# Kernel tuning notes

Measured on AMD Instinct MI355X. Metric: run time of the kernel, lower is better.

## Reference

```python
import jax, jax.numpy as jnp
import numpy as np

H, KV, D, EPS = 32, 8, 128, 1e-6
G = H // KV  # kv groups = 4
ROPE_THETA = 5000000.0


def _rms_norm(x, gamma):
    # x: (..., D)
    return x * jax.lax.rsqrt(jnp.mean(x * x, axis=-1, keepdims=True) + EPS) * gamma


def _rotate_half(x):
    x1, x2 = jnp.split(x, 2, axis=-1)
    return jnp.concatenate([-x2, x1], axis=-1)


def _apply_rope(x, cos, sin):
    # x: (b, h, s, D); cos/sin: (b, s, 1, D) -> (b, 1, s, D)
    cos = jnp.transpose(cos, (0, 2, 1, 3))
    sin = jnp.transpose(sin, (0, 2, 1, 3))
    return x * cos + _rotate_half(x) * sin


def setup_inputs() -> dict:
    key = jax.random.key(0)
    ks = jax.random.split(key, 8)
    b, s, hid = 2, 2048, 2560
    hidden = jax.random.normal(ks[0], (b, s, hid), dtype=jnp.float32)
    # realistic RoPE tables (half-split convention matching _rotate_half)
    inv_freq = 1.0 / (ROPE_THETA ** (np.arange(0, D, 2, dtype=np.float32) / D))  # (D/2,)
    pos = np.arange(s, dtype=np.float32)
    freqs = np.outer(pos, inv_freq)                     # (s, D/2)
    emb = np.concatenate([freqs, freqs], axis=-1)       # (s, D)
    cos = jnp.broadcast_to(jnp.asarray(np.cos(emb))[None, :, None, :], (b, s, 1, D))
    sin = jnp.broadcast_to(jnp.asarray(np.sin(emb))[None, :, None, :], (b, s, 1, D))
    sc = 1.0 / np.sqrt(hid)
    wq = jax.random.normal(ks[1], (H * D, hid), dtype=jnp.float32) * sc
    wk = jax.random.normal(ks[2], (KV * D, hid), dtype=jnp.float32) * sc
    wv = jax.random.normal(ks[3], (KV * D, hid), dtype=jnp.float32) * sc
    wo = jax.random.normal(ks[4], (hid, H * D), dtype=jnp.float32) * (1.0 / np.sqrt(H * D))
    q_gamma = jnp.ones((D,), dtype=jnp.float32)
    k_gamma = jnp.ones((D,), dtype=jnp.float32)
    return {"hidden": hidden, "cos": cos, "sin": sin, "wq": wq, "wk": wk,
            "wv": wv, "wo": wo, "q_gamma": q_gamma, "k_gamma": k_gamma}


def reference(hidden, cos, sin, wq, wk, wv, wo, q_gamma, k_gamma):
    b, s, _ = hidden.shape
    # projections -> (b, heads, s, D)
    q = (hidden @ wq.T).reshape(b, s, H, D).transpose(0, 2, 1, 3)
    k = (hidden @ wk.T).reshape(b, s, KV, D).transpose(0, 2, 1, 3)
    v = (hidden @ wv.T).reshape(b, s, KV, D).transpose(0, 2, 1, 3)
    # QK-RMSNorm over head_dim
    q = _rms_norm(q, q_gamma)
    k = _rms_norm(k, k_gamma)
    # RoPE
    q = _apply_rope(q, cos, sin)
    k = _apply_rope(k, cos, sin)
    new_k, new_v = k, v  # kv cache (no prior cache)
    # GQA attention without materializing expanded K/V
    qg = q.reshape(b, KV, G, s, D)
    scale = 1.0 / np.sqrt(D)
    scores = jnp.einsum('bkgqd,bkld->bkgql', qg, k) * scale  # (b,KV,G,s,s)
    causal = jnp.tril(jnp.ones((s, s), dtype=bool))
    scores = jnp.where(causal, scores, jnp.finfo(scores.dtype).min)
    probs = jax.nn.softmax(scores, axis=-1)
    out = jnp.einsum('bkgql,bkld->bkgqd', probs, v)          # (b,KV,G,s,D)
    out = out.reshape(b, H, s, D).transpose(0, 2, 1, 3).reshape(b, s, H * D)
    return (out @ wo.T, new_k, new_v)
```

## Files before the change

kernel.cpp:

```cpp
#include <hip/hip_runtime.h>
#include <stdint.h>

typedef unsigned short u16;
typedef __attribute__((ext_vector_type(8))) short short8;
typedef __attribute__((ext_vector_type(4))) float f32x4;

#define MFMA_BF16(a,b,c) __builtin_amdgcn_mfma_f32_16x16x32_bf16((a),(b),(c),0,0,0)

#define S_BARRIER()  asm volatile("s_barrier" ::: "memory")
#define WAIT_LGKM0() asm volatile("s_waitcnt lgkmcnt(0)" ::: "memory")
#define WAIT_VM(N)   asm volatile("s_waitcnt vmcnt(" #N ")" ::: "memory")

__device__ __forceinline__ u16 f2bf(float x) {
    uint32_t u = __builtin_bit_cast(uint32_t, x);
    u += 0x7fffu + ((u >> 16) & 1u);
    return (u16)(u >> 16);
}
__device__ __forceinline__ float bf2f(u16 u) {
    return __builtin_bit_cast(float, (uint32_t)u << 16);
}
__device__ __forceinline__ void glds16(const void* g, void* lds) {
    __builtin_amdgcn_global_load_lds((const __attribute__((address_space(1))) void*)g,
                                     (__attribute__((address_space(3))) void*)lds,
                                     16, 0, 0);
}

__device__ __forceinline__ void cvt4(const float* __restrict__ s,
                                     u16* __restrict__ d, int i) {
    float4 v = *(const float4*)(s + i);
    ushort4 o;
    o.x = f2bf(v.x); o.y = f2bf(v.y); o.z = f2bf(v.z); o.w = f2bf(v.w);
    *(ushort4*)(d + i) = o;
}
__global__ __launch_bounds__(256) void cvt_all(
        const float* __restrict__ s0, u16* __restrict__ d0,
        const float* __restrict__ s1, u16* __restrict__ d1,
        const float* __restrict__ s2, u16* __restrict__ d2,
        const float* __restrict__ s3, u16* __restrict__ d3,
        const float* __restrict__ s4, u16* __restrict__ d4)
{
    int i = (blockIdx.x * 256 + threadIdx.x) * 4;
    if      (i < 10485760) cvt4(s0, d0, i);
    else if (i < 20971520) cvt4(s1, d1, i - 10485760);
    else if (i < 23592960) cvt4(s2, d2, i - 20971520);
    else if (i < 26214400) cvt4(s3, d3, i - 23592960);
    else if (i < 36700160) cvt4(s4, d4, i - 26214400);
}

template<int MH, int NH>
__device__ __forceinline__ void mm16(f32x4 (&acc)[8][4],
                                     const short8 (&a)[4][2],
                                     const short8 (&b)[2][2]) {
#pragma unroll
    for (int k2 = 0; k2 < 2; k2++)
#pragma unroll
        for (int mi = 0; mi < 4; mi++)
#pragma unroll
            for (int nj = 0; nj < 2; nj++)
                acc[MH * 4 + mi][NH * 2 + nj] =
                    MFMA_BF16(a[mi][k2], b[nj][k2], acc[MH * 4 + mi][NH * 2 + nj]);
}

template<bool BF16_OUT>
__global__ __launch_bounds__(512, 2) void gemm8(const u16* __restrict__ A,
                                                const u16* __restrict__ B,
                                                void* __restrict__ Cv,
                                                int K, int lda, int ldb, int ldc,
                                                int ntn)
{
    __shared__ __align__(16) u16 Sm[65536];
    const int t = threadIdx.x;
    const int w = t >> 6, l = t & 63;
    const int lrow = l & 15, lk = l >> 4;
    const int wm = w >> 2, wn = w & 3;

    const int nwg = (int)gridDim.x;
    const int cpx = nwg >> 3;
    const int id = (int)blockIdx.x;
    const int sw = (id & 7) * cpx + (id >> 3);
    const int tm = sw / ntn, tn = sw - tm * ntn;
    const int m0 = tm * 256, n0 = tn * 256;

    const int nkt = K >> 6;
    const size_t laneOffA = (size_t)(w * 16 + (l >> 3)) * lda + (((l & 7) ^ (l >> 3)) * 8);
    const size_t laneOffB = (size_t)(w * 16 + (l >> 3)) * ldb + (((l & 7) ^ (l >> 3)) * 8);
    const u16* Ag = A + (size_t)m0 * lda;
    const u16* Bg = B + (size_t)n0 * ldb;

    auto STAGE_A = [&](int kt, int slot, int h) {
#pragma unroll
        for (int j = 0; j < 2; j++)
            glds16(Ag + laneOffA + (size_t)(h * 128 + j * 8) * lda + kt * 64,
                   (char*)Sm + slot * 65536 + h * 16384 + w * 2048 + j * 1024);
    };
    auto STAGE_B = [&](int kt, int slot, int h) {
#pragma unroll
        for (int j = 0; j < 2; j++)
            glds16(Bg + laneOffB + (size_t)(h * 128 + j * 8) * ldb + kt * 64,
                   (char*)Sm + 32768 + slot * 65536 + h * 16384 + w * 2048 + j * 1024);
    };
    auto READ_A = [&](short8 (&a)[4][2], int slot, int rb) {
#pragma unroll
        for (int mi = 0; mi < 4; mi++)
#pragma unroll
            for (int k2 = 0; k2 < 2; k2++) {
                int row = rb + mi * 16 + lrow;
                a[mi][k2] = *(const short8*)&Sm[slot * 32768 + row * 64 +
                                                (((k2 * 4 + lk) ^ (lrow & 7)) * 8)];
            }
    };
    auto READ_B = [&](short8 (&b)[2][2], int slot, int rb) {
#pragma unroll
        for (int nj = 0; nj < 2; nj++)
#pragma unroll
            for (int k2 = 0; k2 < 2; k2++) {
                int row = rb + nj * 16 + lrow;
                b[nj][k2] = *(const short8*)&Sm[slot * 32768 + 16384 + row * 64 +
                                                (((k2 * 4 + lk) ^ (lrow & 7)) * 8)];
            }
    };

    f32x4 acc[8][4];
#pragma unroll
    for (int i = 0; i < 8; i++)
#pragma unroll
        for (int j = 0; j < 4; j++) acc[i][j] = (f32x4){0.f, 0.f, 0.f, 0.f};
    short8 aF0[4][2], aF1[4][2], bF0[2][2], bF1[2][2];

    STAGE_A(0, 0, 0); STAGE_A(0, 0, 1);
    STAGE_B(0, 0, 0); STAGE_B(0, 0, 1);
    const int k1 = (nkt > 1) ? 1 : 0;
    STAGE_A(k1, 1, 0); STAGE_A(k1, 1, 1);
    WAIT_VM(4);
    S_BARRIER();

    for (int kt = 0; kt < nkt; ++kt) {
        const int slot = kt & 1, nslot = slot ^ 1;
        const int ktB = (kt + 1 < nkt) ? kt + 1 : kt;
        const int ktA = (kt + 2 < nkt) ? kt + 2 : kt;
        READ_A(aF0, slot, wm * 128);
        READ_B(bF0, slot, wn * 64);
        STAGE_B(ktB, nslot, 0);
        S_BARRIER();
        WAIT_LGKM0();
        __builtin_amdgcn_sched_barrier(0);
        __builtin_amdgcn_s_setprio(1);
        mm16<0, 0>(acc, aF0, bF0);
        __builtin_amdgcn_s_setprio(0);
        S_BARRIER();
        READ_A(aF1, slot, wm * 128 + 64);
        STAGE_B(ktB, nslot, 1);
        S_BARRIER();
        WAIT_LGKM0();
        __builtin_amdgcn_sched_barrier(0);
        __builtin_amdgcn_s_setprio(1);
        mm16<1, 0>(acc, aF1, bF0);
        __builtin_amdgcn_s_setprio(0);
        S_BARRIER();
        READ_B(bF1, slot, wn * 64 + 32);
        STAGE_A(ktA, slot, 0);
        S_BARRIER();
        WAIT_LGKM0();
        __builtin_amdgcn_sched_barrier(0);
        __builtin_amdgcn_s_setprio(1);
        mm16<1, 1>(acc, aF1, bF1);
        __builtin_amdgcn_s_setprio(0);
        S_BARRIER();
        STAGE_A(ktA, slot, 1);
        S_BARRIER();
        __builtin_amdgcn_s_setprio(1);
        mm16<0, 1>(acc, aF0, bF1);
        __builtin_amdgcn_s_setprio(0);
        WAIT_VM(4);
        S_BARRIER();
    }
    WAIT_VM(0);

#pragma unroll
    for (int mi = 0; mi < 8; mi++) {
#pragma unroll
        for (int r = 0; r < 4; r++) {
            int row = m0 + wm * 128 + mi * 16 + lk * 4 + r;
#pragma unroll
            for (int nj = 0; nj < 4; nj++) {
                int col = n0 + wn * 64 + nj * 16 + lrow;
                float v = acc[mi][nj][r];
                if (BF16_OUT) ((u16*)Cv)[(size_t)row * ldc + col] = f2bf(v);
                else          ((float*)Cv)[(size_t)row * ldc + col] = v;
            }
        }
    }
}

__global__ __launch_bounds__(256) void norm_rope_qk(const u16* __restrict__ qkv,
        const float* __restrict__ cosb, const float* __restrict__ sinb,
        const float* __restrict__ qg, const float* __restrict__ kg,
        u16* __restrict__ qb, u16* __restrict__ kb, float* __restrict__ k_out)
{
    const int idx = blockIdx.x * 4 + (threadIdx.x >> 6);
    const int l = threadIdx.x & 63;
    const int tok = idx / 40, hd = idx - tok * 40;
    const int b = tok >> 11, pos = tok & 2047;
    const u16* row = qkv + (size_t)tok * 6144 + hd * 128;
    ushort2 xr = *(const ushort2*)(row + 2 * l);
    float xa = bf2f(xr.x), xb = bf2f(xr.y);
    float ss = xa * xa + xb * xb;
#pragma unroll
    for (int m = 1; m < 64; m <<= 1) ss += __shfl_xor(ss, m, 64);
    float rn = rsqrtf(ss * (1.0f / 128.0f) + 1e-6f);

    const float* gm = (hd < 32) ? qg : kg;
    float2 g = *(const float2*)(gm + 2 * l);
    float na = xa * rn * g.x, nb = xb * rn * g.y;
    float pa = __shfl_xor(na, 32, 64);
    float pb = __shfl_xor(nb, 32, 64);
    float2 c = *(const float2*)(cosb + (size_t)tok * 128 + 2 * l);
    float2 s = *(const float2*)(sinb + (size_t)tok * 128 + 2 * l);
    float sgn = (l < 32) ? -1.0f : 1.0f;
    float ya = na * c.x + sgn * pa * s.x;
    float yb = nb * c.y + sgn * pb * s.y;
    if (hd < 32) {
        const float qs = 0.12751745f;
        size_t base = (((size_t)b * 32 + hd) * 2048 + pos) * 128;
        ushort2 o; o.x = f2bf(ya * qs); o.y = f2bf(yb * qs);
        *(ushort2*)(qb + base + 2 * l) = o;
    } else {
        int kv = hd - 32;
        size_t base = (((size_t)b * 8 + kv) * 2048 + pos) * 128;
        *(float2*)(k_out + base + 2 * l) = make_float2(ya, yb);
        ushort2 o; o.x = f2bf(ya); o.y = f2bf(yb);
        *(ushort2*)(kb + base + 2 * l) = o;
    }
}

__global__ __launch_bounds__(256) void v_pack(const u16* __restrict__ qkv,
        float* __restrict__ v_out, u16* __restrict__ vtb)
{
    __shared__ __align__(16) u16 T[64 * 128];
    const int pb = blockIdx.x, bkv = blockIdx.y;
    const int b = bkv >> 3, kv = bkv & 7;
    const int p0 = pb * 64;
    const int t = threadIdx.x;
    const int pos = t >> 2, ch4 = t & 3;
    const u16* src = qkv + (size_t)(b * 2048 + p0 + pos) * 6144 + (40 + kv) * 128 + ch4 * 32;
    float* vdst = v_out + ((size_t)bkv * 2048 + p0 + pos) * 128 + ch4 * 32;
#pragma unroll
    for (int j = 0; j < 4; j++) {
        short8 x = *(const short8*)(src + j * 8);
        float4 f0, f1;
        f0.x = bf2f(x[0]); f0.y = bf2f(x[1]); f0.z = bf2f(x[2]); f0.w = bf2f(x[3]);
        f1.x = bf2f(x[4]); f1.y = bf2f(x[5]); f1.z = bf2f(x[6]); f1.w = bf2f(x[7]);
        *(float4*)(vdst + j * 8)     = f0;
        *(float4*)(vdst + j * 8 + 4) = f1;
        int slot = (ch4 * 4 + j) ^ (pos & 7);
        *(short8*)&T[pos * 128 + slot * 8] = x;
    }
    __syncthreads();
    const int d = t & 127, ph = t >> 7;
    u16* obase = vtb + ((size_t)bkv * 128 + d) * 2048 + p0 + ph * 32;
#pragma unroll
    for (int g = 0; g < 4; g++) {
        short8 tv;
#pragma unroll
        for (int jj = 0; jj < 8; jj++) {
            int pp = ph * 32 + g * 8 + jj;
            int slot = (d >> 3) ^ (pp & 7);
            tv[jj] = (short)T[pp * 128 + slot * 8 + (d & 7)];
        }
        *(short8*)(obase + g * 8) = tv;
    }
}

__global__ __launch_bounds__(256, 3) void attn_kernel(const u16* __restrict__ qb,
        const u16* __restrict__ kb, const u16* __restrict__ vtb,
        u16* __restrict__ ao)
{
    __shared__ __align__(16) u16 Ks[64 * 128];
    __shared__ __align__(16) u16 Vs[128 * 64];
    __shared__ __align__(16) u16 Ps[4][32 * 72];

    const int p = (int)blockIdx.x;
    const int g = (p & 7) + ((p >> 5) << 3);
    const int bh = g * 4 + ((p >> 3) & 3);
    const int b = bh >> 5, h = bh & 31;
    const int kvh = h >> 2;
    const int qt = (int)gridDim.y - 1 - (int)blockIdx.y;
    const int q0 = qt * 128;
    const int t = threadIdx.x, w = t >> 6, l = t & 63;
    const int lrow = l & 15, lk = l >> 4;

    const u16* qbase  = qb  + ((size_t)b * 32 + h)  * 2048 * 128;
    const u16* kbase  = kb  + ((size_t)b * 8 + kvh) * 2048 * 128;
    const u16* vtbase = vtb + ((size_t)b * 8 + kvh) * 128 * 2048;

    short8 qf[2][4];
#pragma unroll
    for (int m = 0; m < 2; m++) {
        const u16* qrow = qbase + (size_t)(q0 + w * 32 + m * 16 + lrow) * 128 + lk * 8;
#pragma unroll
        for (int ks = 0; ks < 4; ks++) qf[m][ks] = *(const short8*)(qrow + ks * 32);
    }

    f32x4 o[2][8];
#pragma unroll
    for (int m = 0; m < 2; m++)
#pragma unroll
        for (int i = 0; i < 8; i++) o[m][i] = (f32x4){0.f, 0.f, 0.f, 0.f};
    float lsum[2][4] = {{0.f,0.f,0.f,0.f},{0.f,0.f,0.f,0.f}};

    int kR[4], kG[4], vR[4], vG[4];
#pragma unroll
    for (int i = 0; i < 4; i++) {
        int c = i * 256 + t;
        kR[i] = c >> 4; kG[i] = (c & 15) ^ (kR[i] & 7);
        vR[i] = c >> 3; vG[i] = (c & 7)  ^ (vR[i] & 7);
    }
    char* Ksb = (char*)Ks + w * 1024;
    char* Vsb = (char*)Vs + w * 1024;
    u16* pw = &Ps[w][0];
    const int wrow_max = q0 + w * 32 + 31;

    const int nkt = 2 * qt + 2;
    for (int kt = 0; kt < nkt; kt++) {
        const int kv0 = kt * 64;
        const bool live = (kv0 <= wrow_max);

#pragma unroll
        for (int i = 0; i < 4; i++)
            glds16(kbase + (size_t)(kv0 + kR[i]) * 128 + kG[i] * 8, Ksb + i * 4096);
#pragma unroll
        for (int i = 0; i < 4; i++)
            glds16(vtbase + (size_t)vR[i] * 2048 + kv0 + vG[i] * 8, Vsb + i * 4096);

        WAIT_VM(4);
        S_BARRIER();

        f32x4 s[2][4];
        if (live) {
#pragma unroll
            for (int m = 0; m < 2; m++)
#pragma unroll
                for (int i = 0; i < 4; i++) s[m][i] = (f32x4){0.f, 0.f, 0.f, 0.f};
#pragma unroll
            for (int ks = 0; ks < 4; ks++) {
#pragma unroll
                for (int nt = 0; nt < 4; nt++) {
                    int r = nt * 16 + lrow;
                    int sl = (ks * 4 + lk) ^ (r & 7);
                    short8 kf = *(const short8*)&Ks[r * 128 + sl * 8];
                    s[0][nt] = MFMA_BF16(qf[0][ks], kf, s[0][nt]);
                    s[1][nt] = MFMA_BF16(qf[1][ks], kf, s[1][nt]);
                }
            }
#pragma unroll
            for (int m = 0; m < 2; m++) {
                const int rowbase = q0 + w * 32 + m * 16;
                if (kv0 + 63 > rowbase) {
#pragma unroll
                    for (int nt = 0; nt < 4; nt++) {
                        int cg = kv0 + nt * 16 + lrow;
#pragma unroll
                        for (int r = 0; r < 4; r++)
                            if (cg > rowbase + lk * 4 + r) s[m][nt][r] = -1e30f;
                    }
                }
#pragma unroll
                for (int nt = 0; nt < 4; nt++)
#pragma unroll
                    for (int r = 0; r < 4; r++) {
                        float pv = exp2f(s[m][nt][r]);
                        lsum[m][r] += pv;
                        pw[(m * 16 + lk * 4 + r) * 72 + nt * 16 + lrow] = f2bf(pv);
                    }
            }
            WAIT_LGKM0();
        }

        WAIT_VM(0);
        S_BARRIER();

        if (live) {
#pragma unroll
            for (int k2 = 0; k2 < 2; k2++) {
                short8 pf0 = *(const short8*)&pw[lrow * 72 + k2 * 32 + lk * 8];
                short8 pf1 = *(const short8*)&pw[(16 + lrow) * 72 + k2 * 32 + lk * 8];
#pragma unroll
                for (int nt = 0; nt < 8; nt++) {
                    int rr = nt * 16 + lrow;
                    int sl = (k2 * 4 + lk) ^ (rr & 7);
                    short8 vf = *(const short8*)&Vs[rr * 64 + sl * 8];
                    o[0][nt] = MFMA_BF16(pf0, vf, o[0][nt]);
                    o[1][nt] = MFMA_BF16(pf1, vf, o[1][nt]);
                }
            }
        }
        S_BARRIER();
    }

#pragma unroll
    for (int m = 0; m < 2; m++)
#pragma unroll
        for (int r = 0; r < 4; r++) {
            float v = lsum[m][r];
            v += __shfl_xor(v, 1, 64);
            v += __shfl_xor(v, 2, 64);
            v += __shfl_xor(v, 4, 64);
            v += __shfl_xor(v, 8, 64);
            lsum[m][r] = 1.0f / v;
        }
#pragma unroll
    for (int m = 0; m < 2; m++)
#pragma unroll
        for (int nt = 0; nt < 8; nt++)
#pragma unroll
            for (int r = 0; r < 4; r++) {
                int tok = q0 + w * 32 + m * 16 + lk * 4 + r;
                size_t off = ((size_t)b * 2048 + tok) * 4096 + h * 128 + nt * 16 + lrow;
                ao[off] = f2bf(o[m][nt][r] * lsum[m][r]);
            }
}

extern "C" void kernel_launch(void* const* d_in, const int* in_sizes, int n_in,
                              void* d_out, int out_size, void* d_ws, size_t ws_size,
                              hipStream_t stream)
{
    (void)in_sizes; (void)n_in; (void)out_size; (void)ws_size;
    const float* hidden = (const float*)d_in[0];
    const float* cosb   = (const float*)d_in[1];
    const float* sinb   = (const float*)d_in[2];
    const float* wq     = (const float*)d_in[3];
    const float* wk     = (const float*)d_in[4];
    const float* wv     = (const float*)d_in[5];
    const float* wo     = (const float*)d_in[6];
    const float* qg     = (const float*)d_in[7];
    const float* kg     = (const float*)d_in[8];

    float* out   = (float*)d_out;
    float* k_out = out + (size_t)2 * 2048 * 2560;
    float* v_out = k_out + (size_t)2 * 8 * 2048 * 128;

    u16* hid_b = (u16*)d_ws;
    u16* w_b   = hid_b + 10485760;
    u16* wo_b  = w_b   + 15728640;
    u16* q_b   = wo_b  + 10485760;
    u16* k_b   = q_b   + 16777216;
    u16* vt_b  = k_b   + 4194304;
    u16* qkv_b = vt_b  + 4194304;
    u16* ao_b  = hid_b;

    cvt_all<<<35840, 256, 0, stream>>>(hidden, hid_b, wq, w_b,
                                       wk, w_b + 10485760, wv, w_b + 13107200,
                                       wo, wo_b);

    gemm8<true><<<dim3(384), 512, 0, stream>>>(hid_b, w_b, qkv_b,
                                               2560, 2560, 2560, 6144, 24);
    norm_rope_qk<<<40960, 256, 0, stream>>>(qkv_b, cosb, sinb, qg, kg,
                                            q_b, k_b, k_out);
    v_pack<<<dim3(32, 16), 256, 0, stream>>>(qkv_b, v_out, vt_b);
    attn_kernel<<<dim3(64, 16), 256, 0, stream>>>(q_b, k_b, vt_b, ao_b);
    gemm8<false><<<dim3(160), 512, 0, stream>>>(ao_b, wo_b, out,
                                                4096, 4096, 4096, 2560, 10);
}
```

Measured before the change: 635.7 us.

## Replace output GEMM with simple 128x128 tile kernel and simplify attention loop

Adds a new single-buffered 128x128 tile GEMM (gemm_bt) for the output projection in place of the pipelined gemm8. It also simplifies attention synchronisation to plain __syncthreads with an early continue, and switches from exp2f to __expf with the Q prescale changed from log2e/sqrt(D) to 1/sqrt(D). The new GEMM drops the prefetch pipelining and uses smaller tiles, so load latency is exposed. The attention changes look more like a correctness or simplicity rewrite than a speedup.

```diff
diff --git a/kernel.cpp b/kernel.cpp
--- a/kernel.cpp
+++ b/kernel.cpp
@@ -185,6 +185,78 @@
             for (int nj = 0; nj < 4; nj++) {
                 int col = n0 + wn * 64 + nj * 16 + lrow;
                 float v = acc[mi][nj][r];
+                if (BF16_OUT) ((u16*)Cv)[(size_t)row * ldc + col] = f2bf(v);
+                else          ((float*)Cv)[(size_t)row * ldc + col] = v;
+            }
+        }
+    }
+}
+
+template<bool BF16_OUT>
+__global__ __launch_bounds__(256) void gemm_bt(const u16* __restrict__ A,
+                                               const u16* __restrict__ B,
+                                               void* __restrict__ Cv,
+                                               int K, int lda, int ldb, int ldc)
+{
+    __shared__ __align__(16) u16 As[128 * 64];
+    __shared__ __align__(16) u16 Bs[128 * 64];
+    const int t = threadIdx.x;
+    const int w = t >> 6, l = t & 63;
+    const int m0 = blockIdx.y * 128, n0 = blockIdx.x * 128;
+    const int wm = (w & 1) * 64, wn = (w >> 1) * 64;
+    const int lrow = l & 15, lk = l >> 4;
+
+    f32x4 acc[4][4];
+#pragma unroll
+    for (int i = 0; i < 4; i++)
+#pragma unroll
+        for (int j = 0; j < 4; j++) acc[i][j] = (f32x4){0.f, 0.f, 0.f, 0.f};
+
+    const int row_b = w * 8 + (l >> 3);
+    const int gsw = ((l & 7) ^ (l >> 3)) * 8;
+    const u16* Ap[4]; const u16* Bp[4];
+#pragma unroll
+    for (int i = 0; i < 4; i++) {
+        Ap[i] = A + (size_t)(m0 + row_b + i * 32) * lda + gsw;
+        Bp[i] = B + (size_t)(n0 + row_b + i * 32) * ldb + gsw;
+    }
+    char* Asb = (char*)As + w * 1024;
+    char* Bsb = (char*)Bs + w * 1024;
+
+    for (int k0 = 0; k0 < K; k0 += 64) {
+        __syncthreads();
+#pragma unroll
+        for (int i = 0; i < 4; i++) glds16(Ap[i] + k0, Asb + i * 4096);
+#pragma unroll
+        for (int i = 0; i < 4; i++) glds16(Bp[i] + k0, Bsb + i * 4096);
+        __syncthreads();
+#pragma unroll
+        for (int k2 = 0; k2 < 2; k2++) {
+            const int slb = (k2 * 4 + lk) ^ (lrow & 7);
+            short8 af[4], bf[4];
+#pragma unroll
+            for (int mi = 0; mi < 4; mi++)
+                af[mi] = *(const short8*)&As[(wm + mi * 16 + lrow) * 64 + slb * 8];
+#pragma unroll
+            for (int ni = 0; ni < 4; ni++)
+                bf[ni] = *(const short8*)&Bs[(wn + ni * 16 + lrow) * 64 + slb * 8];
+#pragma unroll
+            for (int mi = 0; mi < 4; mi++)
+#pragma unroll
+                for (int ni = 0; ni < 4; ni++)
+                    acc[mi][ni] = MFMA_BF16(af[mi], bf[ni], acc[mi][ni]);
+        }
+    }
+
+#pragma unroll
+    for (int mi = 0; mi < 4; mi++) {
+#pragma unroll
+        for (int r = 0; r < 4; r++) {
+            int row = m0 + wm + mi * 16 + lk * 4 + r;
+#pragma unroll
+            for (int ni = 0; ni < 4; ni++) {
+                int col = n0 + wn + ni * 16 + lrow;
+                float v = acc[mi][ni][r];
                 if (BF16_OUT) ((u16*)Cv)[(size_t)row * ldc + col] = f2bf(v);
                 else          ((float*)Cv)[(size_t)row * ldc + col] = v;
             }
@@ -220,7 +292,7 @@
     float ya = na * c.x + sgn * pa * s.x;
     float yb = nb * c.y + sgn * pb * s.y;
     if (hd < 32) {
-        const float qs = 0.12751745f;
+        const float qs = 0.08838834764831845f;
         size_t base = (((size_t)b * 32 + hd) * 2048 + pos) * 128;
         ushort2 o; o.x = f2bf(ya * qs); o.y = f2bf(yb * qs);
         *(ushort2*)(qb + base + 2 * l) = o;
@@ -323,78 +395,71 @@
     const int nkt = 2 * qt + 2;
     for (int kt = 0; kt < nkt; kt++) {
         const int kv0 = kt * 64;
-        const bool live = (kv0 <= wrow_max);
-
+        __syncthreads();
 #pragma unroll
         for (int i = 0; i < 4; i++)
             glds16(kbase + (size_t)(kv0 + kR[i]) * 128 + kG[i] * 8, Ksb + i * 4096);
 #pragma unroll
         for (int i = 0; i < 4; i++)
             glds16(vtbase + (size_t)vR[i] * 2048 + kv0 + vG[i] * 8, Vsb + i * 4096);
-
-        WAIT_VM(4);
-        S_BARRIER();
+        __syncthreads();
+
+        if (kv0 > wrow_max) continue;
 
         f32x4 s[2][4];
-        if (live) {
-#pragma unroll
-            for (int m = 0; m < 2; m++)
-#pragma unroll
-                for (int i = 0; i < 4; i++) s[m][i] = (f32x4){0.f, 0.f, 0.f, 0.f};
-#pragma unroll
-            for (int ks = 0; ks < 4; ks++) {
+#pragma unroll
+        for (int m = 0; m < 2; m++)
+#pragma unroll
+            for (int i = 0; i < 4; i++) s[m][i] = (f32x4){0.f, 0.f, 0.f, 0.f};
+#pragma unroll
+        for (int ks = 0; ks < 4; ks++) {
+#pragma unroll
+            for (int nt = 0; nt < 4; nt++) {
+                int r = nt * 16 + lrow;
+                int sl = (ks * 4 + lk) ^ (r & 7);
+                short8 kf = *(const short8*)&Ks[r * 128 + sl * 8];
+                s[0][nt] = MFMA_BF16(qf[0][ks], kf, s[0][nt]);
+                s[1][nt] = MFMA_BF16(qf[1][ks], kf, s[1][nt]);
+            }
+        }
+
+#pragma unroll
+        for (int m = 0; m < 2; m++) {
+            const int rowbase = q0 + w * 32 + m * 16;
+            if (kv0 + 63 > rowbase) {
 #pragma unroll
                 for (int nt = 0; nt < 4; nt++) {
-                    int r = nt * 16 + lrow;
-                    int sl = (ks * 4 + lk) ^ (r & 7);
-                    short8 kf = *(const short8*)&Ks[r * 128 + sl * 8];
-                    s[0][nt] = MFMA_BF16(qf[0][ks], kf, s[0][nt]);
-                    s[1][nt] = MFMA_BF16(qf[1][ks], kf, s[1][nt]);
+                    int cg = kv0 + nt * 16 + lrow;
+#pragma unroll
+                    for (int r = 0; r < 4; r++)
+                        if (cg > rowbase + lk * 4 + r) s[m][nt][r] = -1e30f;
                 }
             }
 #pragma unroll
-            for (int m = 0; m < 2; m++) {
-                const int rowbase = q0 + w * 32 + m * 16;
-                if (kv0 + 63 > rowbase) {
-#pragma unroll
-                    for (int nt = 0; nt < 4; nt++) {
-                        int cg = kv0 + nt * 16 + lrow;
-#pragma unroll
-                        for (int r = 0; r < 4; r++)
-                            if (cg > rowbase + lk * 4 + r) s[m][nt][r] = -1e30f;
-                    }
+            for (int nt = 0; nt < 4; nt++)
+#pragma unroll
+                for (int r = 0; r < 4; r++) {
+                    float pv = __expf(s[m][nt][r]);
+                    s[m][nt][r] = pv;
+                    lsum[m][r] += pv;
+                    pw[(m * 16 + lk * 4 + r) * 72 + nt * 16 + lrow] = f2bf(pv);
                 }
-#pragma unroll
-                for (int nt = 0; nt < 4; nt++)
-#pragma unroll
-                    for (int r = 0; r < 4; r++) {
-                        float pv = exp2f(s[m][nt][r]);
-                        lsum[m][r] += pv;
-                        pw[(m * 16 + lk * 4 + r) * 72 + nt * 16 + lrow] = f2bf(pv);
-                    }
-            }
-            WAIT_LGKM0();
-        }
-
-        WAIT_VM(0);
-        S_BARRIER();
-
-        if (live) {
-#pragma unroll
-            for (int k2 = 0; k2 < 2; k2++) {
-                short8 pf0 = *(const short8*)&pw[lrow * 72 + k2 * 32 + lk * 8];
-                short8 pf1 = *(const short8*)&pw[(16 + lrow) * 72 + k2 * 32 + lk * 8];
-#pragma unroll
-                for (int nt = 0; nt < 8; nt++) {
-                    int rr = nt * 16 + lrow;
-                    int sl = (k2 * 4 + lk) ^ (rr & 7);
-                    short8 vf = *(const short8*)&Vs[rr * 64 + sl * 8];
-                    o[0][nt] = MFMA_BF16(pf0, vf, o[0][nt]);
-                    o[1][nt] = MFMA_BF16(pf1, vf, o[1][nt]);
-                }
-            }
-        }
-        S_BARRIER();
+        }
+        asm volatile("s_waitcnt lgkmcnt(0)" ::: "memory");
+
+#pragma unroll
+        for (int k2 = 0; k2 < 2; k2++) {
+            short8 pf0 = *(const short8*)&pw[lrow * 72 + k2 * 32 + lk * 8];
+            short8 pf1 = *(const short8*)&pw[(16 + lrow) * 72 + k2 * 32 + lk * 8];
+#pragma unroll
+            for (int nt = 0; nt < 8; nt++) {
+                int rr = nt * 16 + lrow;
+                int sl = (k2 * 4 + lk) ^ (rr & 7);
+                short8 vf = *(const short8*)&Vs[rr * 64 + sl * 8];
+                o[0][nt] = MFMA_BF16(pf0, vf, o[0][nt]);
+                o[1][nt] = MFMA_BF16(pf1, vf, o[1][nt]);
+            }
+        }
     }
 
 #pragma unroll
@@ -458,6 +523,6 @@
                                             q_b, k_b, k_out);
     v_pack<<<dim3(32, 16), 256, 0, stream>>>(qkv_b, v_out, vt_b);
     attn_kernel<<<dim3(64, 16), 256, 0, stream>>>(q_b, k_b, vt_b, ao_b);
-    gemm8<false><<<dim3(160), 512, 0, stream>>>(ao_b, wo_b, out,
-                                                4096, 4096, 4096, 2560, 10);
-}
+    gemm_bt<false><<<dim3(20, 32), 256, 0, stream>>>(ao_b, wo_b, out,
+                                                     4096, 4096, 4096, 2560);
+}
```

Measured after the change: 648.9 us. 2.1% more time.
